# Kernel optimization log

Hardware: AMD Instinct MI355X
Metric: run time of the kernel (lower is better)

The kernel has to match this reference:

```python
import jax, jax.numpy as jnp
import numpy as np

N = 16384      # bag size (samples per quantification bag)
DIN = 128      # raw input feature dim
F = 128        # feature_extraction_module.output_size
BINS = 32      # n_bins
H1, H2 = 1024, 512
NC = 10        # n_classes
SIGMA = 100.0  # soft-histogram steepness


def setup_inputs() -> dict:
    key = jax.random.key(0)
    ks = jax.random.split(key, 6)
    w = lambda k, shp: (jax.random.normal(k, shp, jnp.float32) * 0.02)
    return {
        "x": jax.random.normal(ks[0], (N, DIN), jnp.float32),
        "W_feat": w(ks[1], (DIN, F)),
        "b_feat": jnp.zeros((F,), jnp.float32),
        "W1": w(ks[2], (F * BINS, H1)),
        "b1": jnp.zeros((H1,), jnp.float32),
        "W2": w(ks[3], (H1, H2)),
        "b2": jnp.zeros((H2,), jnp.float32),
        "W3": w(ks[4], (H2, NC)),
        "b3": jnp.zeros((NC,), jnp.float32),
    }


def _soft_histogram(s):
    # s: [N, F] values in (0,1). Uniform bins over [0,1].
    delta = 1.0 / BINS
    centers = (jnp.arange(BINS, dtype=s.dtype) + 0.5) * delta  # [BINS]
    d = s[:, :, None] - centers  # [N, F, BINS]  (fusion target)
    soft = jax.nn.sigmoid(SIGMA * (d + 0.5 * delta)) - jax.nn.sigmoid(SIGMA * (d - 0.5 * delta))
    return jnp.mean(soft, axis=0)  # [F, BINS] normalized counts


def reference(x, W_feat, b_feat, W1, b1, W2, b2, W3, b3):
    feats = x @ W_feat + b_feat                 # [N, F] feature extraction
    s = jax.nn.sigmoid(feats)                   # Sigmoid layer -> (0,1)
    hist = _soft_histogram(s).reshape(F * BINS) # differentiable histogram, flattened
    h = jax.nn.leaky_relu(hist @ W1 + b1)       # Linear + LeakyReLU (Dropout p=0 -> identity)
    h = jax.nn.leaky_relu(h @ W2 + b2)
    logits = h @ W3 + b3                        # [NC]
    return jax.nn.softmax(logits, axis=0)       # Softmax(dim=0) over classes
```

## Files before the change

kernel.cpp:

```cpp
#include <hip/hip_runtime.h>
#include <math.h>

#define N_SAMP 16384
#define DIN 128
#define FDIM 128
#define BINS 32
#define NEDGE 33
#define CELLS (FDIM * NEDGE)
#define H1 1024
#define H2 512
#define NC 10

#define K1_BLOCKS 512
#define K1_ROWS 32
#define K1_THREADS 512
#define XS_STRIDE 132

#define K3_BLOCKS 256

#define EXP_3_125 22.7598950f

__device__ __forceinline__ float fast_sigmoid_from_t(float t) {
    return __builtin_amdgcn_rcpf(1.f + t);
}
__device__ __forceinline__ float lrelu(float x) { return x > 0.f ? x : 0.01f * x; }

__global__ __launch_bounds__(K1_THREADS, 4) void k1_feat_hist(
    const float* __restrict__ x, const float* __restrict__ Wf,
    const float* __restrict__ bf, float* __restrict__ E_part)
{
    __shared__ float xs[K1_ROWS * XS_STRIDE];
    const int t = threadIdx.x;
    const int blk = blockIdx.x;
    const int row0 = blk * K1_ROWS;

    #pragma unroll
    for (int i = 0; i < 2; ++i) {
        const int idx = t + i * K1_THREADS;
        const int r = idx >> 5, c4 = (idx & 31) << 2;
        *(float4*)&xs[r * XS_STRIDE + c4] =
            *(const float4*)(x + (size_t)(row0 + r) * DIN + c4);
    }
    __syncthreads();

    const int tc = t & 31, tr = t >> 5;
    const int f0 = tc * 4, r0 = tr * 2;

    float4 acc0 = {0,0,0,0}, acc1 = {0,0,0,0};
    #pragma unroll 2
    for (int d = 0; d < DIN; d += 4) {
        const float4 xa = *(const float4*)&xs[r0 * XS_STRIDE + d];
        const float4 xb = *(const float4*)&xs[(r0 + 1) * XS_STRIDE + d];
        const float* wp = Wf + d * FDIM + f0;
        const float4 w0 = *(const float4*)(wp);
        const float4 w1 = *(const float4*)(wp + FDIM);
        const float4 w2 = *(const float4*)(wp + 2 * FDIM);
        const float4 w3 = *(const float4*)(wp + 3 * FDIM);
        acc0.x = fmaf(xa.x, w0.x, acc0.x); acc0.y = fmaf(xa.x, w0.y, acc0.y);
        acc0.z = fmaf(xa.x, w0.z, acc0.z); acc0.w = fmaf(xa.x, w0.w, acc0.w);
        acc0.x = fmaf(xa.y, w1.x, acc0.x); acc0.y = fmaf(xa.y, w1.y, acc0.y);
        acc0.z = fmaf(xa.y, w1.z, acc0.z); acc0.w = fmaf(xa.y, w1.w, acc0.w);
        acc0.x = fmaf(xa.z, w2.x, acc0.x); acc0.y = fmaf(xa.z, w2.y, acc0.y);
        acc0.z = fmaf(xa.z, w2.z, acc0.z); acc0.w = fmaf(xa.z, w2.w, acc0.w);
        acc0.x = fmaf(xa.w, w3.x, acc0.x); acc0.y = fmaf(xa.w, w3.y, acc0.y);
        acc0.z = fmaf(xa.w, w3.z, acc0.z); acc0.w = fmaf(xa.w, w3.w, acc0.w);
        acc1.x = fmaf(xb.x, w0.x, acc1.x); acc1.y = fmaf(xb.x, w0.y, acc1.y);
        acc1.z = fmaf(xb.x, w0.z, acc1.z); acc1.w = fmaf(xb.x, w0.w, acc1.w);
        acc1.x = fmaf(xb.y, w1.x, acc1.x); acc1.y = fmaf(xb.y, w1.y, acc1.y);
        acc1.z = fmaf(xb.y, w1.z, acc1.z); acc1.w = fmaf(xb.y, w1.w, acc1.w);
        acc1.x = fmaf(xb.z, w2.x, acc1.x); acc1.y = fmaf(xb.z, w2.y, acc1.y);
        acc1.z = fmaf(xb.z, w2.z, acc1.z); acc1.w = fmaf(xb.z, w2.w, acc1.w);
        acc1.x = fmaf(xb.w, w3.x, acc1.x); acc1.y = fmaf(xb.w, w3.y, acc1.y);
        acc1.z = fmaf(xb.w, w3.z, acc1.z); acc1.w = fmaf(xb.w, w3.w, acc1.w);
    }

    const float4 bv = *(const float4*)(bf + f0);
    float4 s0, s1;
    s0.x = fast_sigmoid_from_t(__expf(-(acc0.x + bv.x)));
    s0.y = fast_sigmoid_from_t(__expf(-(acc0.y + bv.y)));
    s0.z = fast_sigmoid_from_t(__expf(-(acc0.z + bv.z)));
    s0.w = fast_sigmoid_from_t(__expf(-(acc0.w + bv.w)));
    s1.x = fast_sigmoid_from_t(__expf(-(acc1.x + bv.x)));
    s1.y = fast_sigmoid_from_t(__expf(-(acc1.y + bv.y)));
    s1.z = fast_sigmoid_from_t(__expf(-(acc1.z + bv.z)));
    s1.w = fast_sigmoid_from_t(__expf(-(acc1.w + bv.w)));

    __syncthreads();
    *(float4*)&xs[r0 * XS_STRIDE + f0] = s0;
    *(float4*)&xs[(r0 + 1) * XS_STRIDE + f0] = s1;
    __syncthreads();

    const int feat = t & 127;
    const int eg = t >> 7;
    const int estart = (eg == 0) ? 0 : eg * 8 + 1;
    const int ne = (eg == 0) ? 9 : 8;
    const float c0 = 3.125f * (float)estart;

    float locE[9];
    #pragma unroll
    for (int j = 0; j < 9; ++j) locE[j] = 0.f;

    for (int r = 0; r < K1_ROWS; ++r) {
        const float s = xs[r * XS_STRIDE + feat];
        float tt = __expf(c0 - 100.f * s);
        #pragma unroll
        for (int j = 0; j < 9; ++j) {
            locE[j] += fast_sigmoid_from_t(tt);
            tt *= EXP_3_125;
        }
    }

    float* dst = E_part + (size_t)blk * CELLS + feat * NEDGE + estart;
    for (int j = 0; j < ne; ++j) dst[j] = locE[j];
}

__global__ __launch_bounds__(256) void k3_h1(
    const float* __restrict__ E_part, const float* __restrict__ W1,
    float* __restrict__ h1_part)
{
    const int b = blockIdx.x, t = threadIdx.x;
    const int f = b >> 1, bin0 = (b & 1) * 16;
    const int c0 = f * NEDGE + bin0;

    float4 w[16];
    #pragma unroll
    for (int k = 0; k < 16; ++k)
        w[k] = *(const float4*)(W1 + (size_t)(b * 16 + k) * H1 + t * 4);

    __shared__ float Ered[8 * 17];
    __shared__ float hl[17];
    const int cw = t & 31, g = t >> 5;
    if (cw < 17) {
        const float* p0 = E_part + (size_t)(g * 64) * CELLS + c0 + cw;
        float a0 = 0, a1 = 0, a2 = 0, a3 = 0;
        #pragma unroll 4
        for (int p = 0; p < 64; p += 4) {
            a0 += p0[(size_t)(p + 0) * CELLS];
            a1 += p0[(size_t)(p + 1) * CELLS];
            a2 += p0[(size_t)(p + 2) * CELLS];
            a3 += p0[(size_t)(p + 3) * CELLS];
        }
        Ered[g * 17 + cw] = (a0 + a1) + (a2 + a3);
    }
    __syncthreads();
    if (t < 17) {
        float s = 0.f;
        #pragma unroll
        for (int g2 = 0; g2 < 8; ++g2) s += Ered[g2 * 17 + t];
        hl[t] = s;
    }
    __syncthreads();

    float4 acc = {0,0,0,0};
    #pragma unroll
    for (int k = 0; k < 16; ++k) {
        const float h = (hl[k] - hl[k + 1]) * (1.f / (float)N_SAMP);
        acc.x = fmaf(h, w[k].x, acc.x);
        acc.y = fmaf(h, w[k].y, acc.y);
        acc.z = fmaf(h, w[k].z, acc.z);
        acc.w = fmaf(h, w[k].w, acc.w);
    }
    *(float4*)(h1_part + (size_t)b * H1 + t * 4) = acc;
}

__global__ __launch_bounds__(128) void k5_h2(
    const float* __restrict__ h1_part, const float* __restrict__ b1,
    const float* __restrict__ W2, float* __restrict__ h2_part)
{
    const int b = blockIdx.x, t = threadIdx.x;

    float4 w[8];
    #pragma unroll
    for (int k = 0; k < 8; ++k)
        w[k] = *(const float4*)(W2 + (size_t)(b * 8 + k) * H2 + t * 4);

    __shared__ float hred[8 * 16];
    __shared__ float hv[8];
    const int col = t & 7, q = t >> 3;
    {
        const float* p0 = h1_part + (size_t)(q * 16) * H1 + b * 8 + col;
        float a0 = 0, a1 = 0, a2 = 0, a3 = 0;
        #pragma unroll
        for (int p = 0; p < 16; p += 4) {
            a0 += p0[(size_t)(p + 0) * H1];
            a1 += p0[(size_t)(p + 1) * H1];
            a2 += p0[(size_t)(p + 2) * H1];
            a3 += p0[(size_t)(p + 3) * H1];
        }
        hred[col * 16 + q] = (a0 + a1) + (a2 + a3);
    }
    __syncthreads();
    if (t < 8) {
        float s = 0.f;
        #pragma unroll
        for (int q2 = 0; q2 < 16; ++q2) s += hred[t * 16 + q2];
        hv[t] = lrelu(s + b1[b * 8 + t]);
    }
    __syncthreads();

    float4 acc = {0,0,0,0};
    #pragma unroll
    for (int k = 0; k < 8; ++k) {
        const float h = hv[k];
        acc.x = fmaf(h, w[k].x, acc.x);
        acc.y = fmaf(h, w[k].y, acc.y);
        acc.z = fmaf(h, w[k].z, acc.z);
        acc.w = fmaf(h, w[k].w, acc.w);
    }
    *(float4*)(h2_part + (size_t)b * H2 + t * 4) = acc;
}

__global__ __launch_bounds__(512) void k6_final(
    const float* __restrict__ h2_part, const float* __restrict__ b2,
    const float* __restrict__ W3, const float* __restrict__ b3,
    float* __restrict__ out)
{
    const int t = threadIdx.x;
    float a0 = 0, a1 = 0, a2 = 0, a3 = 0;
    #pragma unroll 8
    for (int p = 0; p < 128; p += 4) {
        a0 += h2_part[(size_t)(p + 0) * H2 + t];
        a1 += h2_part[(size_t)(p + 1) * H2 + t];
        a2 += h2_part[(size_t)(p + 2) * H2 + t];
        a3 += h2_part[(size_t)(p + 3) * H2 + t];
    }
    const float h2v = lrelu(((a0 + a1) + (a2 + a3)) + b2[t]);

    float lc[NC];
    #pragma unroll
    for (int c = 0; c < NC; ++c) lc[c] = h2v * W3[t * NC + c];
    #pragma unroll
    for (int off = 32; off >= 1; off >>= 1) {
        #pragma unroll
        for (int c = 0; c < NC; ++c) lc[c] += __shfl_down(lc[c], off, 64);
    }

    __shared__ float wsum[8][NC];
    if ((t & 63) == 0) {
        #pragma unroll
        for (int c = 0; c < NC; ++c) wsum[t >> 6][c] = lc[c];
    }
    __syncthreads();

    if (t == 0) {
        float logits[NC];
        float m = -1e30f;
        #pragma unroll
        for (int c = 0; c < NC; ++c) {
            float v = b3[c];
            for (int ww = 0; ww < 8; ++ww) v += wsum[ww][c];
            logits[c] = v;
            m = fmaxf(m, v);
        }
        float ssum = 0.f;
        #pragma unroll
        for (int c = 0; c < NC; ++c) { logits[c] = __expf(logits[c] - m); ssum += logits[c]; }
        const float inv = 1.f / ssum;
        #pragma unroll
        for (int c = 0; c < NC; ++c) out[c] = logits[c] * inv;
    }
}

extern "C" void kernel_launch(void* const* d_in, const int* in_sizes, int n_in,
                              void* d_out, int out_size, void* d_ws, size_t ws_size,
                              hipStream_t stream)
{
    const float* x  = (const float*)d_in[0];
    const float* Wf = (const float*)d_in[1];
    const float* bf = (const float*)d_in[2];
    const float* W1 = (const float*)d_in[3];
    const float* b1 = (const float*)d_in[4];
    const float* W2 = (const float*)d_in[5];
    const float* b2 = (const float*)d_in[6];
    const float* W3 = (const float*)d_in[7];
    const float* b3 = (const float*)d_in[8];
    float* out = (float*)d_out;

    float* ws      = (float*)d_ws;
    float* E_part  = ws;
    float* h1_part = E_part + (size_t)K1_BLOCKS * CELLS;
    float* h2_part = h1_part + (size_t)K3_BLOCKS * H1;

    k1_feat_hist<<<K1_BLOCKS, K1_THREADS, 0, stream>>>(x, Wf, bf, E_part);
    k3_h1<<<K3_BLOCKS, 256, 0, stream>>>(E_part, W1, h1_part);
    k5_h2<<<128, 128, 0, stream>>>(h1_part, b1, W2, h2_part);
    k6_final<<<1, 512, 0, stream>>>(h2_part, b2, W3, b3, out);
}
```

Before: 133.4 us.

## Skip saturated sigmoid chains per wave, halve rows per block, add partial reduce

Each histogram wave now checks whether all its lanes sit far below or far above its edge range. If so it skips the exp/reciprocal chain, either adding nothing or counting the row as fully saturated. The feature kernel processes 16 rows per block over twice as many blocks with a higher occupancy hint. A new reduction kernel collapses the per-block edge partials into 32 groups so the first MLP layer reads fewer partials. The cost is twice the partial-buffer traffic, an extra kernel launch, and a small approximation for the skipped near-saturated terms.

Measured after the change: 152.3 us. 1.14x slower.

```diff
diff --git a/kernel.cpp b/kernel.cpp
--- a/kernel.cpp
+++ b/kernel.cpp
@@ -11,21 +11,32 @@
 #define H2 512
 #define NC 10
 
-#define K1_BLOCKS 512
-#define K1_ROWS 32
+#define K1_BLOCKS 1024
+#define K1_ROWS 16
 #define K1_THREADS 512
 #define XS_STRIDE 132
 
+#define K2_GROUPS 32
 #define K3_BLOCKS 256
 
 #define EXP_3_125 22.7598950f
 
-__device__ __forceinline__ float fast_sigmoid_from_t(float t) {
+__device__ __forceinline__ float sig_from_t(float t) {
     return __builtin_amdgcn_rcpf(1.f + t);
 }
 __device__ __forceinline__ float lrelu(float x) { return x > 0.f ? x : 0.01f * x; }
 
-__global__ __launch_bounds__(K1_THREADS, 4) void k1_feat_hist(
+template <int NE>
+__device__ __forceinline__ void sig_chain(float z0neg, float* locE) {
+    float tt = __expf(z0neg);
+    #pragma unroll
+    for (int j = 0; j < NE; ++j) {
+        locE[j] += sig_from_t(tt);
+        tt *= EXP_3_125;
+    }
+}
+
+__global__ __launch_bounds__(K1_THREADS, 8) void k1_feat_hist(
     const float* __restrict__ x, const float* __restrict__ Wf,
     const float* __restrict__ bf, float* __restrict__ E_part)
 {
@@ -34,60 +45,44 @@
     const int blk = blockIdx.x;
     const int row0 = blk * K1_ROWS;
 
-    #pragma unroll
-    for (int i = 0; i < 2; ++i) {
-        const int idx = t + i * K1_THREADS;
-        const int r = idx >> 5, c4 = (idx & 31) << 2;
+    {
+        const int r = t >> 5, c4 = (t & 31) << 2;
         *(float4*)&xs[r * XS_STRIDE + c4] =
             *(const float4*)(x + (size_t)(row0 + r) * DIN + c4);
     }
     __syncthreads();
 
     const int tc = t & 31, tr = t >> 5;
-    const int f0 = tc * 4, r0 = tr * 2;
-
-    float4 acc0 = {0,0,0,0}, acc1 = {0,0,0,0};
-    #pragma unroll 2
+    const int f0 = tc * 4;
+
+    float4 acc = {0, 0, 0, 0};
+    #pragma unroll 4
     for (int d = 0; d < DIN; d += 4) {
-        const float4 xa = *(const float4*)&xs[r0 * XS_STRIDE + d];
-        const float4 xb = *(const float4*)&xs[(r0 + 1) * XS_STRIDE + d];
+        const float4 xa = *(const float4*)&xs[tr * XS_STRIDE + d];
         const float* wp = Wf + d * FDIM + f0;
         const float4 w0 = *(const float4*)(wp);
         const float4 w1 = *(const float4*)(wp + FDIM);
         const float4 w2 = *(const float4*)(wp + 2 * FDIM);
         const float4 w3 = *(const float4*)(wp + 3 * FDIM);
-        acc0.x = fmaf(xa.x, w0.x, acc0.x); acc0.y = fmaf(xa.x, w0.y, acc0.y);
-        acc0.z = fmaf(xa.x, w0.z, acc0.z); acc0.w = fmaf(xa.x, w0.w, acc0.w);
-        acc0.x = fmaf(xa.y, w1.x, acc0.x); acc0.y = fmaf(xa.y, w1.y, acc0.y);
-        acc0.z = fmaf(xa.y, w1.z, acc0.z); acc0.w = fmaf(xa.y, w1.w, acc0.w);
-        acc0.x = fmaf(xa.z, w2.x, acc0.x); acc0.y = fmaf(xa.z, w2.y, acc0.y);
-        acc0.z = fmaf(xa.z, w2.z, acc0.z); acc0.w = fmaf(xa.z, w2.w, acc0.w);
-        acc0.x = fmaf(xa.w, w3.x, acc0.x); acc0.y = fmaf(xa.w, w3.y, acc0.y);
-        acc0.z = fmaf(xa.w, w3.z, acc0.z); acc0.w = fmaf(xa.w, w3.w, acc0.w);
-        acc1.x = fmaf(xb.x, w0.x, acc1.x); acc1.y = fmaf(xb.x, w0.y, acc1.y);
-        acc1.z = fmaf(xb.x, w0.z, acc1.z); acc1.w = fmaf(xb.x, w0.w, acc1.w);
-        acc1.x = fmaf(xb.y, w1.x, acc1.x); acc1.y = fmaf(xb.y, w1.y, acc1.y);
-        acc1.z = fmaf(xb.y, w1.z, acc1.z); acc1.w = fmaf(xb.y, w1.w, acc1.w);
-        acc1.x = fmaf(xb.z, w2.x, acc1.x); acc1.y = fmaf(xb.z, w2.y, acc1.y);
-        acc1.z = fmaf(xb.z, w2.z, acc1.z); acc1.w = fmaf(xb.z, w2.w, acc1.w);
-        acc1.x = fmaf(xb.w, w3.x, acc1.x); acc1.y = fmaf(xb.w, w3.y, acc1.y);
-        acc1.z = fmaf(xb.w, w3.z, acc1.z); acc1.w = fmaf(xb.w, w3.w, acc1.w);
+        acc.x = fmaf(xa.x, w0.x, acc.x); acc.y = fmaf(xa.x, w0.y, acc.y);
+        acc.z = fmaf(xa.x, w0.z, acc.z); acc.w = fmaf(xa.x, w0.w, acc.w);
+        acc.x = fmaf(xa.y, w1.x, acc.x); acc.y = fmaf(xa.y, w1.y, acc.y);
+        acc.z = fmaf(xa.y, w1.z, acc.z); acc.w = fmaf(xa.y, w1.w, acc.w);
+        acc.x = fmaf(xa.z, w2.x, acc.x); acc.y = fmaf(xa.z, w2.y, acc.y);
+        acc.z = fmaf(xa.z, w2.z, acc.z); acc.w = fmaf(xa.z, w2.w, acc.w);
+        acc.x = fmaf(xa.w, w3.x, acc.x); acc.y = fmaf(xa.w, w3.y, acc.y);
+        acc.z = fmaf(xa.w, w3.z, acc.z); acc.w = fmaf(xa.w, w3.w, acc.w);
     }
 
     const float4 bv = *(const float4*)(bf + f0);
-    float4 s0, s1;
-    s0.x = fast_sigmoid_from_t(__expf(-(acc0.x + bv.x)));
-    s0.y = fast_sigmoid_from_t(__expf(-(acc0.y + bv.y)));
-    s0.z = fast_sigmoid_from_t(__expf(-(acc0.z + bv.z)));
-    s0.w = fast_sigmoid_from_t(__expf(-(acc0.w + bv.w)));
-    s1.x = fast_sigmoid_from_t(__expf(-(acc1.x + bv.x)));
-    s1.y = fast_sigmoid_from_t(__expf(-(acc1.y + bv.y)));
-    s1.z = fast_sigmoid_from_t(__expf(-(acc1.z + bv.z)));
-    s1.w = fast_sigmoid_from_t(__expf(-(acc1.w + bv.w)));
-
-    __syncthreads();
-    *(float4*)&xs[r0 * XS_STRIDE + f0] = s0;
-    *(float4*)&xs[(r0 + 1) * XS_STRIDE + f0] = s1;
+    float4 sv;
+    sv.x = sig_from_t(__expf(-(acc.x + bv.x)));
+    sv.y = sig_from_t(__expf(-(acc.y + bv.y)));
+    sv.z = sig_from_t(__expf(-(acc.z + bv.z)));
+    sv.w = sig_from_t(__expf(-(acc.w + bv.w)));
+
+    __syncthreads();
+    *(float4*)&xs[tr * XS_STRIDE + f0] = sv;
     __syncthreads();
 
     const int feat = t & 127;
@@ -95,27 +90,48 @@
     const int estart = (eg == 0) ? 0 : eg * 8 + 1;
     const int ne = (eg == 0) ? 9 : 8;
     const float c0 = 3.125f * (float)estart;
+    const float cLast = 3.125f * (float)(estart + ne - 1);
 
     float locE[9];
     #pragma unroll
     for (int j = 0; j < 9; ++j) locE[j] = 0.f;
+    float cnt = 0.f;
 
     for (int r = 0; r < K1_ROWS; ++r) {
-        const float s = xs[r * XS_STRIDE + feat];
-        float tt = __expf(c0 - 100.f * s);
-        #pragma unroll
-        for (int j = 0; j < 9; ++j) {
-            locE[j] += fast_sigmoid_from_t(tt);
-            tt *= EXP_3_125;
+        const float z100 = 100.f * xs[r * XS_STRIDE + feat];
+        if (__all(z100 - c0 <= -15.f)) {
+        } else if (__all(z100 - cLast >= 15.f)) {
+            cnt += 1.f;
+        } else {
+            if (eg == 0) sig_chain<9>(c0 - z100, locE);
+            else         sig_chain<8>(c0 - z100, locE);
         }
     }
 
     float* dst = E_part + (size_t)blk * CELLS + feat * NEDGE + estart;
-    for (int j = 0; j < ne; ++j) dst[j] = locE[j];
+    for (int j = 0; j < ne; ++j) dst[j] = locE[j] + cnt;
+}
+
+__global__ __launch_bounds__(256) void k2_reduce(
+    const float* __restrict__ E_part, float* __restrict__ E32)
+{
+    const int cell = blockIdx.x * 256 + threadIdx.x;
+    if (cell >= CELLS) return;
+    const int g = blockIdx.y;
+    const float* p = E_part + (size_t)g * 32 * CELLS + cell;
+    float a0 = 0, a1 = 0, a2 = 0, a3 = 0;
+    #pragma unroll
+    for (int q = 0; q < 32; q += 4) {
+        a0 += p[(size_t)(q + 0) * CELLS];
+        a1 += p[(size_t)(q + 1) * CELLS];
+        a2 += p[(size_t)(q + 2) * CELLS];
+        a3 += p[(size_t)(q + 3) * CELLS];
+    }
+    E32[g * CELLS + cell] = (a0 + a1) + (a2 + a3);
 }
 
 __global__ __launch_bounds__(256) void k3_h1(
-    const float* __restrict__ E_part, const float* __restrict__ W1,
+    const float* __restrict__ E32, const float* __restrict__ W1,
     float* __restrict__ h1_part)
 {
     const int b = blockIdx.x, t = threadIdx.x;
@@ -127,31 +143,22 @@
     for (int k = 0; k < 16; ++k)
         w[k] = *(const float4*)(W1 + (size_t)(b * 16 + k) * H1 + t * 4);
 
-    __shared__ float Ered[8 * 17];
     __shared__ float hl[17];
-    const int cw = t & 31, g = t >> 5;
-    if (cw < 17) {
-        const float* p0 = E_part + (size_t)(g * 64) * CELLS + c0 + cw;
+    if (t < 17) {
+        const float* p = E32 + c0 + t;
         float a0 = 0, a1 = 0, a2 = 0, a3 = 0;
-        #pragma unroll 4
-        for (int p = 0; p < 64; p += 4) {
-            a0 += p0[(size_t)(p + 0) * CELLS];
-            a1 += p0[(size_t)(p + 1) * CELLS];
-            a2 += p0[(size_t)(p + 2) * CELLS];
-            a3 += p0[(size_t)(p + 3) * CELLS];
-        }
-        Ered[g * 17 + cw] = (a0 + a1) + (a2 + a3);
-    }
-    __syncthreads();
-    if (t < 17) {
-        float s = 0.f;
-        #pragma unroll
-        for (int g2 = 0; g2 < 8; ++g2) s += Ered[g2 * 17 + t];
-        hl[t] = s;
-    }
-    __syncthreads();
-
-    float4 acc = {0,0,0,0};
+        #pragma unroll
+        for (int g = 0; g < 32; g += 4) {
+            a0 += p[(size_t)(g + 0) * CELLS];
+            a1 += p[(size_t)(g + 1) * CELLS];
+            a2 += p[(size_t)(g + 2) * CELLS];
+            a3 += p[(size_t)(g + 3) * CELLS];
+        }
+        hl[t] = (a0 + a1) + (a2 + a3);
+    }
+    __syncthreads();
+
+    float4 acc = {0, 0, 0, 0};
     #pragma unroll
     for (int k = 0; k < 16; ++k) {
         const float h = (hl[k] - hl[k + 1]) * (1.f / (float)N_SAMP);
@@ -198,7 +205,7 @@
     }
     __syncthreads();
 
-    float4 acc = {0,0,0,0};
+    float4 acc = {0, 0, 0, 0};
     #pragma unroll
     for (int k = 0; k < 8; ++k) {
         const float h = hv[k];
@@ -278,11 +285,13 @@
 
     float* ws      = (float*)d_ws;
     float* E_part  = ws;
-    float* h1_part = E_part + (size_t)K1_BLOCKS * CELLS;
+    float* E32     = E_part + (size_t)K1_BLOCKS * CELLS;
+    float* h1_part = E32 + (size_t)K2_GROUPS * CELLS;
     float* h2_part = h1_part + (size_t)K3_BLOCKS * H1;
 
     k1_feat_hist<<<K1_BLOCKS, K1_THREADS, 0, stream>>>(x, Wf, bf, E_part);
-    k3_h1<<<K3_BLOCKS, 256, 0, stream>>>(E_part, W1, h1_part);
+    k2_reduce<<<dim3(17, K2_GROUPS), 256, 0, stream>>>(E_part, E32);
+    k3_h1<<<K3_BLOCKS, 256, 0, stream>>>(E32, W1, h1_part);
     k5_h2<<<128, 128, 0, stream>>>(h1_part, b1, W2, h2_part);
     k6_final<<<1, 512, 0, stream>>>(h2_part, b2, W3, b3, out);
 }
```
